# Kernel optimization log

Hardware: AMD Instinct MI355X
Metric: run time of the kernel (lower is better)

Reference implementation:

```python
import jax, jax.numpy as jnp
import numpy as np
from string import ascii_letters as ABC

N = 12
DIM = 2 ** N
_s = 1.0 / np.sqrt(2.0)
# measurement-basis rotations for X, Y, Z
U_BASIS = jnp.asarray(np.stack([
    np.array([[1, 1], [1, -1]]) * _s,
    np.array([[1, -1j], [1, 1j]]) * _s,
    np.eye(2),
]), dtype=jnp.complex64)


def build_H(params_x, params_zz):
    """Dense transverse-field Ising Hamiltonian: sum_i x_i X_i + sum_i zz_i Z_i Z_{i+1}."""
    basis = jnp.arange(DIM)
    bits = (basis[:, None] >> jnp.arange(N)[None, :]) & 1          # (DIM, N)
    signs = (1 - 2 * bits).astype(jnp.float32)                      # Z eigenvalues
    zz_diag = (signs[:, :-1] * signs[:, 1:]) @ params_zz            # (DIM,)
    flips = basis[:, None] ^ (1 << jnp.arange(N))[None, :]          # (DIM, N)
    rows = jnp.repeat(basis, N)
    cols = flips.reshape(-1)
    vals = jnp.tile(params_x, DIM).astype(jnp.complex64)
    H = jnp.zeros((DIM, DIM), jnp.complex64).at[rows, cols].add(vals)
    return H + jnp.diag(zz_diag.astype(jnp.complex64))


def setup_inputs() -> dict:
    key = jax.random.key(0)
    k1, k2, k3, k4, k5 = jax.random.split(key, 5)
    return {
        "initial_state": 0,
        "ts": jax.random.uniform(k1, (8,), dtype=jnp.float32),
        "pauli_obs": jax.random.randint(k2, (32, N), 0, 3),
        "indices": jax.random.randint(k3, (8, 32, 256), 0, DIM),
        "params_x": jax.random.normal(k4, (N,), dtype=jnp.float32),
        "params_zz": jax.random.normal(k5, (N - 1,), dtype=jnp.float32),
    }


def reference(initial_state, ts, pauli_obs, indices, params_x, params_zz):
    H = build_H(params_x, params_zz)
    rots = U_BASIS[pauli_obs]                    # (B, N, 2, 2)
    ops = [rots[:, i] for i in range(N)]
    subs = ','.join([ABC[1:1 + N]] + [f'a{ABC[1 + N + i]}{ABC[1 + i]}' for i in range(N)]) \
        + '->a' + ABC[1 + N:1 + 2 * N]
    B = pauli_obs.shape[0]

    def one_t(args):
        t, idx = args
        U = jax.scipy.linalg.expm((-1j) * t.astype(jnp.complex64) * H)
        fs = U[:, initial_state].reshape([2] * N)          # state tensor
        rot_state = jnp.einsum(subs, fs, *ops)             # (B, 2, ..., 2)
        probs = jnp.abs(rot_state.reshape(B, DIM)) ** 2    # (B, DIM)
        return jnp.take_along_axis(probs, idx, axis=1)     # (B, shots)

    return jax.lax.map(one_t, (ts, indices))               # (T, B, shots)
```

## Files before the change

kernel.cpp:

```cpp
#include <hip/hip_runtime.h>
#include <math.h>

#define QN 12
#define QDIM 4096
#define CHEB_TOL 1e-3f
#define LSZ (QDIM + 2 * (QDIM / 16))

template <int CTRL>
__device__ __forceinline__ float dppf(float x) {
    int v = __builtin_amdgcn_update_dpp(0, __float_as_int(x), CTRL, 0xF, 0xF, false);
    return __int_as_float(v);
}
#define DPP_QX1 0xB1
#define DPP_QX2 0x4E
#define DPP_QX3 0x1B
#define DPP_HM  0x141
#define DPP_R8  0x128
__device__ __forceinline__ float dpp_x1(float x) { return dppf<DPP_QX1>(x); }
__device__ __forceinline__ float dpp_x2(float x) { return dppf<DPP_QX2>(x); }
__device__ __forceinline__ float dpp_x4(float x) { return dppf<DPP_HM>(dppf<DPP_QX3>(x)); }
__device__ __forceinline__ float dpp_x8(float x) { return dppf<DPP_R8>(x); }

__global__ __launch_bounds__(1024) void evolve_kernel(
    const int* __restrict__ init_state,
    const float* __restrict__ ts,
    const float* __restrict__ params_x,
    const float* __restrict__ params_zz,
    float2* __restrict__ psi_out)
{
    __shared__ float2 bufA[LSZ];
    __shared__ float2 bufB[LSZ];
    __shared__ float  Jc[128];
    __shared__ float  suLDS[160];
    __shared__ int    dsh;

    const int tid = threadIdx.x;
    const int tI  = blockIdx.x;
    const float t = ts[tI];
    const int g0 = tid * 4;
    const int h0 = g0 >> 4;
    const int l0 = g0 + 2 * h0;

    if (tid < 160) suLDS[tid] = 0.f;

    float xj[QN];
    float bound = 0.f;
#pragma unroll
    for (int j = 0; j < QN; ++j) { xj[j] = params_x[j]; bound += fabsf(xj[j]); }
    float zz[QN - 1];
#pragma unroll
    for (int i = 0; i < QN - 1; ++i) { zz[i] = params_zz[i]; bound += fabsf(zz[i]); }

    float dg[4];
#pragma unroll
    for (int k = 0; k < 4; ++k) {
        const int g = g0 + k;
        float dv = 0.f;
#pragma unroll
        for (int i = 0; i < QN - 1; ++i) {
            const int flip = ((g >> i) ^ (g >> (i + 1))) & 1;
            dv += zz[i] * (1.0f - 2.0f * (float)flip);
        }
        dg[k] = dv;
    }

    const float theta = t * bound;
    int dmax = (int)ceilf(theta + 5.0f * cbrtf(theta)) + 6;
    if (dmax < 8) dmax = 8;
    if (dmax > 126) dmax = 126;

    {
        const int M = dmax + 24;
        const double th = (double)fmaxf(theta, 1e-6f);
        const double invth = 1.0 / th;
        double jkp1 = 0.0, jk = 1e-30, mine = 0.0, nrm = 0.0, suf = 0.0, su_own = 0.0;
        for (int k = M; k >= 0; --k) {
            suf += fabs(jk);
            if (k == tid) { mine = jk; su_own = suf; }
            if (k == 0) nrm += jk;
            else if ((k & 1) == 0) nrm += 2.0 * jk;
            const double jkm1 = (2.0 * (double)k * invth) * jk - jkp1;
            jkp1 = jk; jk = jkm1;
            if (fabs(jk) > 1e250) {
                jk *= 1e-250; jkp1 *= 1e-250; mine *= 1e-250;
                nrm *= 1e-250; suf *= 1e-250; su_own *= 1e-250;
            }
        }
        const double anrm = fabs(nrm);
        if (tid <= dmax) Jc[tid] = (float)(mine / nrm);
        if (tid < 160) suLDS[tid] = (float)(su_own / anrm);
    }

    const int is = init_state[0];
    const float inv_s = 1.0f / bound;

    float2 tp[4];
    float2 tpp[4];
    float2 acc[4];
#pragma unroll
    for (int k = 0; k < 4; ++k) {
        const float v = (g0 + k == is) ? 1.0f : 0.0f;
        tp[k]  = make_float2(v, 0.f);
        tpp[k] = make_float2(0.f, 0.f);
        bufA[l0 + k] = tp[k];
    }
    __syncthreads();

    if (tid < 64) {
        const bool p0 = suLDS[tid + 1] < CHEB_TOL;
        const bool p1 = suLDS[tid + 65] < CHEB_TOL;
        const unsigned long long b0 = __ballot(p0);
        const unsigned long long b1 = __ballot(p1);
        if (tid == 0) {
            int dd;
            if (b0) dd = __ffsll(b0) - 1;
            else if (b1) dd = 64 + __ffsll(b1) - 1;
            else dd = dmax;
            if (dd < 2) dd = 2;
            if (dd > dmax) dd = dmax;
            dsh = dd;
        }
    }
    __syncthreads();
    const int d = dsh;

#pragma unroll
    for (int k = 0; k < 4; ++k) {
        acc[k] = make_float2(Jc[0] * tp[k].x, 0.f);
    }

    float2* cur = bufA;
    float2* nxt = bufB;

    for (int k = 1; k <= d; ++k) {
        float hr[4], hi[4];
#pragma unroll
        for (int kk = 0; kk < 4; ++kk) {
            hr[kk] = dg[kk] * tp[kk].x + xj[0] * tp[kk ^ 1].x + xj[1] * tp[kk ^ 2].x;
            hi[kk] = dg[kk] * tp[kk].y + xj[0] * tp[kk ^ 1].y + xj[1] * tp[kk ^ 2].y;
            hr[kk] += xj[2] * dpp_x1(tp[kk].x);
            hi[kk] += xj[2] * dpp_x1(tp[kk].y);
            hr[kk] += xj[3] * dpp_x2(tp[kk].x);
            hi[kk] += xj[3] * dpp_x2(tp[kk].y);
            hr[kk] += xj[4] * dpp_x4(tp[kk].x);
            hi[kk] += xj[4] * dpp_x4(tp[kk].y);
            hr[kk] += xj[5] * dpp_x8(tp[kk].x);
            hi[kk] += xj[5] * dpp_x8(tp[kk].y);
        }
#pragma unroll
        for (int j = 6; j < QN; ++j) {
            const int gx = g0 ^ (1 << j);
            const int hx = h0 ^ (1 << (j - 4));
            const float4* p = (const float4*)(cur + gx + 2 * hx);
            const float4 a = p[0];
            const float4 b = p[1];
            hr[0] += xj[j] * a.x; hi[0] += xj[j] * a.y;
            hr[1] += xj[j] * a.z; hi[1] += xj[j] * a.w;
            hr[2] += xj[j] * b.x; hi[2] += xj[j] * b.y;
            hr[3] += xj[j] * b.z; hi[3] += xj[j] * b.w;
        }

        const float f = (k == 1) ? inv_s : 2.0f * inv_s;
        float2 tn[4];
#pragma unroll
        for (int kk = 0; kk < 4; ++kk) {
            tn[kk] = make_float2(f * hr[kk] - tpp[kk].x, f * hi[kk] - tpp[kk].y);
        }

        const float Jk2 = 2.0f * Jc[k];
        float cr = 0.f, ci = 0.f;
        switch (k & 3) {
            case 0: cr =  Jk2; break;
            case 1: ci = -Jk2; break;
            case 2: cr = -Jk2; break;
            case 3: ci =  Jk2; break;
        }
#pragma unroll
        for (int kk = 0; kk < 4; ++kk) {
            acc[kk].x += cr * tn[kk].x - ci * tn[kk].y;
            acc[kk].y += cr * tn[kk].y + ci * tn[kk].x;
        }

        float4* w = (float4*)(nxt + l0);
        w[0] = make_float4(tn[0].x, tn[0].y, tn[1].x, tn[1].y);
        w[1] = make_float4(tn[2].x, tn[2].y, tn[3].x, tn[3].y);
        __syncthreads();

#pragma unroll
        for (int kk = 0; kk < 4; ++kk) { tpp[kk] = tp[kk]; tp[kk] = tn[kk]; }
        float2* tmp = cur; cur = nxt; nxt = tmp;
    }

    float4* o = (float4*)(psi_out + tI * QDIM + g0);
    o[0] = make_float4(acc[0].x, acc[0].y, acc[1].x, acc[1].y);
    o[1] = make_float4(acc[2].x, acc[2].y, acc[3].x, acc[3].y);
}

__global__ __launch_bounds__(512) void measure_kernel(
    const float2* __restrict__ psi,
    const int* __restrict__ pauli_obs,
    const int* __restrict__ indices,
    float* __restrict__ out)
{
    __shared__ float2 st[QDIM];
    const int blk = blockIdx.x;
    const int tI = blk >> 5;
    const int b  = blk & 31;

    const float4* src = (const float4*)(psi + tI * QDIM);
    float4* dst = (float4*)st;
    for (int i = threadIdx.x; i < QDIM / 2; i += 512) dst[i] = src[i];
    __syncthreads();

    const float s = 0.70710678118654752440f;
    for (int q = 0; q < QN; ++q) {
        const int p = pauli_obs[b * QN + (QN - 1 - q)];
        if (p == 2) continue;
        const int mask = 1 << q;
        for (int it = threadIdx.x; it < QDIM / 2; it += 512) {
            const int gl = ((it & ~(mask - 1)) << 1) | (it & (mask - 1));
            const int gh = gl | mask;
            const float2 a  = st[gl];
            const float2 c2 = st[gh];
            float2 r0, r1;
            if (p == 0) {
                r0 = make_float2(s * (a.x + c2.x), s * (a.y + c2.y));
                r1 = make_float2(s * (a.x - c2.x), s * (a.y - c2.y));
            } else {
                r0 = make_float2(s * (a.x + c2.y), s * (a.y - c2.x));
                r1 = make_float2(s * (a.x - c2.y), s * (a.y + c2.x));
            }
            st[gl] = r0;
            st[gh] = r1;
        }
        __syncthreads();
    }

    if (threadIdx.x < 256) {
        const int oi = (tI * 32 + b) * 256 + threadIdx.x;
        const int idx = indices[oi];
        const float2 v = st[idx];
        out[oi] = v.x * v.x + v.y * v.y;
    }
}

extern "C" void kernel_launch(void* const* d_in, const int* in_sizes, int n_in,
                              void* d_out, int out_size, void* d_ws, size_t ws_size,
                              hipStream_t stream) {
    const int*   init_state = (const int*)d_in[0];
    const float* ts         = (const float*)d_in[1];
    const int*   pauli_obs  = (const int*)d_in[2];
    const int*   indices    = (const int*)d_in[3];
    const float* params_x   = (const float*)d_in[4];
    const float* params_zz  = (const float*)d_in[5];
    float*  out = (float*)d_out;
    float2* psi = (float2*)d_ws;

    hipLaunchKernelGGL(evolve_kernel, dim3(8), dim3(1024), 0, stream,
                       init_state, ts, params_x, params_zz, psi);
    hipLaunchKernelGGL(measure_kernel, dim3(8 * 32), dim3(512), 0, stream,
                       psi, pauli_obs, indices, out);
}
```

Measured before the change: 120.4 us.

## Give each thread 16 amplitudes, unroll Chebyshev loop by two, loosen truncation

The evolve kernel now runs 256 threads per block, and each thread holds 16 amplitudes in registers instead of 4. Four qubit flips are applied in-register, four use DPP lane swizzles, and only four go through shared memory, with wider vector loads. The Chebyshev recurrence is unrolled by two so the previous and current vectors swap roles without register copies, and the phase branch becomes odd/even FMAs. The Chebyshev tail tolerance is doubled, so fewer terms are summed. Each thread now uses more registers and there are fewer waves to hide latency, and the looser tolerance slightly lowers accuracy.

```diff
diff --git a/kernel.cpp b/kernel.cpp
--- a/kernel.cpp
+++ b/kernel.cpp
@@ -3,7 +3,7 @@
 
 #define QN 12
 #define QDIM 4096
-#define CHEB_TOL 1e-3f
+#define CHEB_TOL 2e-3f
 #define LSZ (QDIM + 2 * (QDIM / 16))
 
 template <int CTRL>
@@ -21,15 +21,72 @@
 __device__ __forceinline__ float dpp_x4(float x) { return dppf<DPP_HM>(dppf<DPP_QX3>(x)); }
 __device__ __forceinline__ float dpp_x8(float x) { return dppf<DPP_R8>(x); }
 
-__global__ __launch_bounds__(1024) void evolve_kernel(
+#define CHEB_STEP(T1, T2, CURB, NXTB, KVAL, FVAL, ODD)                        \
+    {                                                                          \
+        const int   k_ = (KVAL);                                               \
+        const float f_ = (FVAL);                                               \
+        float hr[16], hi[16];                                                  \
+        _Pragma("unroll")                                                      \
+        for (int e = 0; e < 16; ++e) {                                         \
+            hr[e] = dg[e] * T1[e].x + xj[0] * T1[e ^ 1].x                      \
+                  + xj[1] * T1[e ^ 2].x + xj[2] * T1[e ^ 4].x                  \
+                  + xj[3] * T1[e ^ 8].x;                                       \
+            hi[e] = dg[e] * T1[e].y + xj[0] * T1[e ^ 1].y                      \
+                  + xj[1] * T1[e ^ 2].y + xj[2] * T1[e ^ 4].y                  \
+                  + xj[3] * T1[e ^ 8].y;                                       \
+            hr[e] += xj[4] * dpp_x1(T1[e].x);  hi[e] += xj[4] * dpp_x1(T1[e].y); \
+            hr[e] += xj[5] * dpp_x2(T1[e].x);  hi[e] += xj[5] * dpp_x2(T1[e].y); \
+            hr[e] += xj[6] * dpp_x4(T1[e].x);  hi[e] += xj[6] * dpp_x4(T1[e].y); \
+            hr[e] += xj[7] * dpp_x8(T1[e].x);  hi[e] += xj[7] * dpp_x8(T1[e].y); \
+        }                                                                      \
+        _Pragma("unroll")                                                      \
+        for (int j = 8; j < QN; ++j) {                                         \
+            const int gx = g0 ^ (1 << j);                                      \
+            const int hx = tid ^ (1 << (j - 4));                               \
+            const float4* q4 = (const float4*)((CURB) + gx + 2 * hx);          \
+            float4 nbv[8];                                                     \
+            _Pragma("unroll")                                                  \
+            for (int m = 0; m < 8; ++m) nbv[m] = q4[m];                        \
+            _Pragma("unroll")                                                  \
+            for (int m = 0; m < 8; ++m) {                                      \
+                hr[2 * m]     += xj[j] * nbv[m].x;                             \
+                hi[2 * m]     += xj[j] * nbv[m].y;                             \
+                hr[2 * m + 1] += xj[j] * nbv[m].z;                             \
+                hi[2 * m + 1] += xj[j] * nbv[m].w;                             \
+            }                                                                  \
+        }                                                                      \
+        const float Jk2 = 2.0f * Jc[k_];                                       \
+        const float c_  = (k_ & 2) ? Jk2 : -Jk2;                               \
+        _Pragma("unroll")                                                      \
+        for (int e = 0; e < 16; ++e) {                                         \
+            const float tnx = f_ * hr[e] - T2[e].x;                            \
+            const float tny = f_ * hi[e] - T2[e].y;                            \
+            T2[e].x = tnx; T2[e].y = tny;                                      \
+            if (ODD) {                                                         \
+                acc[e].x = fmaf(-c_, tny, acc[e].x);                           \
+                acc[e].y = fmaf( c_, tnx, acc[e].y);                           \
+            } else {                                                           \
+                acc[e].x = fmaf(-c_, tnx, acc[e].x);                           \
+                acc[e].y = fmaf(-c_, tny, acc[e].y);                           \
+            }                                                                  \
+        }                                                                      \
+        float4* w_ = (float4*)((NXTB) + l0);                                   \
+        _Pragma("unroll")                                                      \
+        for (int m = 0; m < 8; ++m)                                            \
+            w_[m] = make_float4(T2[2 * m].x, T2[2 * m].y,                      \
+                                T2[2 * m + 1].x, T2[2 * m + 1].y);             \
+        __syncthreads();                                                       \
+    }
+
+__global__ __launch_bounds__(256) void evolve_kernel(
     const int* __restrict__ init_state,
     const float* __restrict__ ts,
     const float* __restrict__ params_x,
     const float* __restrict__ params_zz,
     float2* __restrict__ psi_out)
 {
-    __shared__ float2 bufA[LSZ];
-    __shared__ float2 bufB[LSZ];
+    __shared__ __align__(16) float2 bufA[LSZ];
+    __shared__ __align__(16) float2 bufB[LSZ];
     __shared__ float  Jc[128];
     __shared__ float  suLDS[160];
     __shared__ int    dsh;
@@ -37,9 +94,8 @@
     const int tid = threadIdx.x;
     const int tI  = blockIdx.x;
     const float t = ts[tI];
-    const int g0 = tid * 4;
-    const int h0 = g0 >> 4;
-    const int l0 = g0 + 2 * h0;
+    const int g0 = tid * 16;
+    const int l0 = g0 + 2 * tid;
 
     if (tid < 160) suLDS[tid] = 0.f;
 
@@ -51,17 +107,17 @@
 #pragma unroll
     for (int i = 0; i < QN - 1; ++i) { zz[i] = params_zz[i]; bound += fabsf(zz[i]); }
 
-    float dg[4];
-#pragma unroll
-    for (int k = 0; k < 4; ++k) {
-        const int g = g0 + k;
+    float dg[16];
+#pragma unroll
+    for (int e = 0; e < 16; ++e) {
+        const int g = g0 + e;
         float dv = 0.f;
 #pragma unroll
         for (int i = 0; i < QN - 1; ++i) {
             const int flip = ((g >> i) ^ (g >> (i + 1))) & 1;
             dv += zz[i] * (1.0f - 2.0f * (float)flip);
         }
-        dg[k] = dv;
+        dg[e] = dv;
     }
 
     const float theta = t * bound;
@@ -94,15 +150,21 @@
     const int is = init_state[0];
     const float inv_s = 1.0f / bound;
 
-    float2 tp[4];
-    float2 tpp[4];
-    float2 acc[4];
-#pragma unroll
-    for (int k = 0; k < 4; ++k) {
-        const float v = (g0 + k == is) ? 1.0f : 0.0f;
-        tp[k]  = make_float2(v, 0.f);
-        tpp[k] = make_float2(0.f, 0.f);
-        bufA[l0 + k] = tp[k];
+    float2 ta[16];
+    float2 tb[16];
+    float2 acc[16];
+#pragma unroll
+    for (int e = 0; e < 16; ++e) {
+        const float v = (g0 + e == is) ? 1.0f : 0.0f;
+        ta[e] = make_float2(v, 0.f);
+        tb[e] = make_float2(0.f, 0.f);
+    }
+    {
+        float4* w0 = (float4*)(bufA + l0);
+#pragma unroll
+        for (int m = 0; m < 8; ++m)
+            w0[m] = make_float4(ta[2 * m].x, ta[2 * m].y,
+                                ta[2 * m + 1].x, ta[2 * m + 1].y);
     }
     __syncthreads();
 
@@ -125,75 +187,24 @@
     const int d = dsh;
 
 #pragma unroll
-    for (int k = 0; k < 4; ++k) {
-        acc[k] = make_float2(Jc[0] * tp[k].x, 0.f);
-    }
-
-    float2* cur = bufA;
-    float2* nxt = bufB;
-
-    for (int k = 1; k <= d; ++k) {
-        float hr[4], hi[4];
-#pragma unroll
-        for (int kk = 0; kk < 4; ++kk) {
-            hr[kk] = dg[kk] * tp[kk].x + xj[0] * tp[kk ^ 1].x + xj[1] * tp[kk ^ 2].x;
-            hi[kk] = dg[kk] * tp[kk].y + xj[0] * tp[kk ^ 1].y + xj[1] * tp[kk ^ 2].y;
-            hr[kk] += xj[2] * dpp_x1(tp[kk].x);
-            hi[kk] += xj[2] * dpp_x1(tp[kk].y);
-            hr[kk] += xj[3] * dpp_x2(tp[kk].x);
-            hi[kk] += xj[3] * dpp_x2(tp[kk].y);
-            hr[kk] += xj[4] * dpp_x4(tp[kk].x);
-            hi[kk] += xj[4] * dpp_x4(tp[kk].y);
-            hr[kk] += xj[5] * dpp_x8(tp[kk].x);
-            hi[kk] += xj[5] * dpp_x8(tp[kk].y);
-        }
-#pragma unroll
-        for (int j = 6; j < QN; ++j) {
-            const int gx = g0 ^ (1 << j);
-            const int hx = h0 ^ (1 << (j - 4));
-            const float4* p = (const float4*)(cur + gx + 2 * hx);
-            const float4 a = p[0];
-            const float4 b = p[1];
-            hr[0] += xj[j] * a.x; hi[0] += xj[j] * a.y;
-            hr[1] += xj[j] * a.z; hi[1] += xj[j] * a.w;
-            hr[2] += xj[j] * b.x; hi[2] += xj[j] * b.y;
-            hr[3] += xj[j] * b.z; hi[3] += xj[j] * b.w;
-        }
-
-        const float f = (k == 1) ? inv_s : 2.0f * inv_s;
-        float2 tn[4];
-#pragma unroll
-        for (int kk = 0; kk < 4; ++kk) {
-            tn[kk] = make_float2(f * hr[kk] - tpp[kk].x, f * hi[kk] - tpp[kk].y);
-        }
-
-        const float Jk2 = 2.0f * Jc[k];
-        float cr = 0.f, ci = 0.f;
-        switch (k & 3) {
-            case 0: cr =  Jk2; break;
-            case 1: ci = -Jk2; break;
-            case 2: cr = -Jk2; break;
-            case 3: ci =  Jk2; break;
-        }
-#pragma unroll
-        for (int kk = 0; kk < 4; ++kk) {
-            acc[kk].x += cr * tn[kk].x - ci * tn[kk].y;
-            acc[kk].y += cr * tn[kk].y + ci * tn[kk].x;
-        }
-
-        float4* w = (float4*)(nxt + l0);
-        w[0] = make_float4(tn[0].x, tn[0].y, tn[1].x, tn[1].y);
-        w[1] = make_float4(tn[2].x, tn[2].y, tn[3].x, tn[3].y);
-        __syncthreads();
-
-#pragma unroll
-        for (int kk = 0; kk < 4; ++kk) { tpp[kk] = tp[kk]; tp[kk] = tn[kk]; }
-        float2* tmp = cur; cur = nxt; nxt = tmp;
+    for (int e = 0; e < 16; ++e) acc[e] = make_float2(Jc[0] * ta[e].x, 0.f);
+
+    CHEB_STEP(ta, tb, bufA, bufB, 1, inv_s, true);
+    const float f2 = 2.0f * inv_s;
+    int k = 2;
+    for (; k + 1 <= d; k += 2) {
+        CHEB_STEP(tb, ta, bufB, bufA, k,     f2, false);
+        CHEB_STEP(ta, tb, bufA, bufB, k + 1, f2, true);
+    }
+    if (k <= d) {
+        CHEB_STEP(tb, ta, bufB, bufA, k, f2, false);
     }
 
     float4* o = (float4*)(psi_out + tI * QDIM + g0);
-    o[0] = make_float4(acc[0].x, acc[0].y, acc[1].x, acc[1].y);
-    o[1] = make_float4(acc[2].x, acc[2].y, acc[3].x, acc[3].y);
+#pragma unroll
+    for (int m = 0; m < 8; ++m)
+        o[m] = make_float4(acc[2 * m].x, acc[2 * m].y,
+                           acc[2 * m + 1].x, acc[2 * m + 1].y);
 }
 
 __global__ __launch_bounds__(512) void measure_kernel(
@@ -256,7 +267,7 @@
     float*  out = (float*)d_out;
     float2* psi = (float2*)d_ws;
 
-    hipLaunchKernelGGL(evolve_kernel, dim3(8), dim3(1024), 0, stream,
+    hipLaunchKernelGGL(evolve_kernel, dim3(8), dim3(256), 0, stream,
                        init_state, ts, params_x, params_zz, psi);
     hipLaunchKernelGGL(measure_kernel, dim3(8 * 32), dim3(512), 0, stream,
                        psi, pauli_obs, indices, out);
```

Result: no change. 120.2 us (-0.2%).
